# Performance work log

Hardware: AMD Instinct MI355X
Metric: run time of the kernel (lower is better)

## Reference

```python
import jax, jax.numpy as jnp
import numpy as np

S, B, E, H, FFN = 2048, 2, 1024, 16, 4096
HD = E // H
EPS = 1e-5

def setup_inputs() -> dict:
    key = jax.random.key(0)
    ks = jax.random.split(key, 10)
    w = lambda k, shape: 0.02 * jax.random.normal(k, shape, dtype=jnp.float32)
    inp = {
        "x": jax.random.normal(ks[0], (S, B, E), dtype=jnp.float32),
        "key_padding_mask": jax.random.randint(ks[1], (B, S), 0, 2) == 1,
        # attention projections, stored as (in, out) so y = x @ W + b
        "Wq": w(ks[2], (E, E)), "bq": jnp.zeros((E,), jnp.float32),
        "Wk": w(ks[3], (E, E)), "bk": jnp.zeros((E,), jnp.float32),
        "Wv": w(ks[4], (E, E)), "bv": jnp.zeros((E,), jnp.float32),
        "Wo": w(ks[5], (E, E)), "bo": jnp.zeros((E,), jnp.float32),
        "ln1_g": jnp.ones((E,), jnp.float32), "ln1_b": jnp.zeros((E,), jnp.float32),
        "W1": w(ks[6], (E, FFN)), "b1": jnp.zeros((FFN,), jnp.float32),
        "W2": w(ks[7], (FFN, E)), "b2": jnp.zeros((E,), jnp.float32),
        "ln2_g": jnp.ones((E,), jnp.float32), "ln2_b": jnp.zeros((E,), jnp.float32),
    }
    return inp

def layer_norm(x, g, b):
    m = jnp.mean(x, axis=-1, keepdims=True)
    v = jnp.mean(jnp.square(x - m), axis=-1, keepdims=True)
    return (x - m) * jax.lax.rsqrt(v + EPS) * g + b

def reference(x, key_padding_mask, Wq, bq, Wk, bk, Wv, bv, Wo, bo,
              ln1_g, ln1_b, W1, b1, W2, b2, ln2_g, ln2_b):
    # ---- self-attention (post-LN, normalize_before=False) ----
    residual = x  # (S, B, E)
    scaling = 1.0 / jnp.sqrt(jnp.float32(HD))
    q = (scaling * (x @ Wq + bq)).reshape(S, B, H, HD)
    k = (x @ Wk + bk).reshape(S, B, H, HD)
    v = (x @ Wv + bv).reshape(S, B, H, HD)
    # scores: (B, H, S_q, S_k)
    attn = jnp.einsum('ibhd,jbhd->bhij', q, k)
    attn = jnp.where(key_padding_mask[:, None, None, :], -jnp.inf, attn)
    attn = jax.nn.softmax(attn, axis=-1)
    out = jnp.einsum('bhij,jbhd->ibhd', attn, v).reshape(S, B, E)
    h = out @ Wo + bo
    h = layer_norm(residual + h, ln1_g, ln1_b)
    # ---- FFN ----
    residual = h
    f = jax.nn.relu(h @ W1 + b1) @ W2 + b2
    h = layer_norm(residual + f, ln2_g, ln2_b)
    # torch clamps only when inf/nan appear; finite inputs here so no-op
    return h
```

## Files before the change

kernel.cpp:

```cpp
#include <hip/hip_runtime.h>
#include <hip/hip_bf16.h>

using u16 = unsigned short;
using u32 = unsigned int;

constexpr int S_LEN = 2048, BATCH = 2, EMB = 1024, NHEAD = 16, HDIM = 64, FFN_DIM = 4096;
constexpr int NTOK = S_LEN * BATCH;
constexpr int QKV_N = 3 * EMB;
#define QSCALE 0.18033688011112042f

typedef __attribute__((ext_vector_type(4))) float f32x4;
typedef __attribute__((ext_vector_type(8))) short short8;
typedef __attribute__((ext_vector_type(8))) __bf16 bf16x8;
typedef __attribute__((ext_vector_type(8))) u16 ushort8;
typedef __attribute__((ext_vector_type(4))) u16 u16x4;
typedef __attribute__((ext_vector_type(2))) u32 u32x2;

typedef const __attribute__((address_space(1))) u16 gu16;
typedef __attribute__((address_space(3))) u16 lu16;

__device__ __forceinline__ u16 f2bf(float f) {
  u32 u = __builtin_bit_cast(u32, f);
  u32 r = u + 0x7fffu + ((u >> 16) & 1u);
  return (u16)(r >> 16);
}
__device__ __forceinline__ float bf2f(u16 u) {
  return __builtin_bit_cast(float, (u32)u << 16);
}

__device__ __forceinline__ f32x4 mfma16(short8 a, short8 b, f32x4 c) {
  return __builtin_amdgcn_mfma_f32_16x16x32_bf16(
      __builtin_bit_cast(bf16x8, a), __builtin_bit_cast(bf16x8, b), c, 0, 0, 0);
}

__device__ __forceinline__ void gload16(const u16* g, u16* l) {
  __builtin_amdgcn_global_load_lds((gu16*)g, (lu16*)l, 16, 0, 0);
}

__device__ __forceinline__ u32 cvtpk(float lo, float hi) {
  u32 r;
  asm("v_cvt_pk_bf16_f32 %0, %1, %2" : "=v"(r) : "v"(lo), "v"(hi));
  return r;
}

__global__ __launch_bounds__(256) void k_cvt_bf16(const float* __restrict__ in,
                                                  u16* __restrict__ out, int n) {
  int i = (blockIdx.x * 256 + threadIdx.x) * 8;
  if (i >= n) return;
  float4 a = *(const float4*)(in + i);
  float4 b = *(const float4*)(in + i + 4);
  ushort8 o;
  o[0] = f2bf(a.x); o[1] = f2bf(a.y); o[2] = f2bf(a.z); o[3] = f2bf(a.w);
  o[4] = f2bf(b.x); o[5] = f2bf(b.y); o[6] = f2bf(b.z); o[7] = f2bf(b.w);
  *(ushort8*)(out + i) = o;
}

__global__ __launch_bounds__(256) void k_transpose_w(const float* __restrict__ in,
                                                     u16* __restrict__ out, int R, int C,
                                                     float scale) {
  __shared__ float t[32][33];
  int c0 = blockIdx.x * 32, r0 = blockIdx.y * 32;
  int tx = threadIdx.x & 31, ty = threadIdx.x >> 5;
#pragma unroll
  for (int i = 0; i < 4; ++i)
    t[ty + i * 8][tx] = in[(r0 + ty + i * 8) * C + c0 + tx];
  __syncthreads();
#pragma unroll
  for (int i = 0; i < 4; ++i)
    out[(c0 + ty + i * 8) * R + r0 + tx] = f2bf(t[tx][ty + i * 8] * scale);
}

__global__ void k_bias_cat(const float* __restrict__ bq, const float* __restrict__ bk,
                           const float* __restrict__ bv, float* __restrict__ bcat) {
  int i = blockIdx.x * 256 + threadIdx.x;
  float v = (i < 1024) ? bq[i] * QSCALE : (i < 2048 ? bk[i - 1024] : bv[i - 2048]);
  bcat[i] = v;
}

__global__ void k_mask_f(const int* __restrict__ m, float* __restrict__ mf, int n) {
  int i = blockIdx.x * 256 + threadIdx.x;
  if (i < n) mf[i] = m[i] ? -1e30f : 0.f;
}

__global__ void k_transpose_v(const u16* __restrict__ qkvb, u16* __restrict__ vT) {
  __shared__ u16 t[64][65];
  int s0 = blockIdx.x * 64;
  int bh = blockIdx.y;
  int b = bh >> 4, h = bh & 15;
  int tx = threadIdx.x, ty = threadIdx.y;
#pragma unroll
  for (int i = 0; i < 16; ++i) {
    int s = i * 4 + ty;
    t[s][tx] = qkvb[((s0 + s) * BATCH + b) * QKV_N + 2048 + h * HDIM + tx];
  }
  __syncthreads();
#pragma unroll
  for (int i = 0; i < 16; ++i) {
    int d = i * 4 + ty;
    vT[(bh * HDIM + d) * S_LEN + s0 + tx] = t[tx][d];
  }
}

template <int NS, bool RELU>
__global__ __launch_bounds__(256, 4) void k_gemm128(
    const u16* __restrict__ A, const u16* __restrict__ Bt,
    const float* __restrict__ bias, u16* __restrict__ C,
    u16* __restrict__ P1, u16* __restrict__ P2, u16* __restrict__ P3,
    int M, int N, int K, int nbx) {
  __shared__ u16 As[2][128 * 32];
  __shared__ u16 Bs[2][128 * 32];
  int tid = threadIdx.x;
  int lane = tid & 63;
  int lm = lane & 15, lg = lane >> 4;
  int w = tid >> 6;
  int wm = w >> 1, wn = w & 1;

  int cpx = gridDim.x >> 3;
  int nw = (blockIdx.x & 7) * cpx + (blockIdx.x >> 3);
  int nb = gridDim.x / NS;
  int slice = nw / nb;
  int t0 = nw - slice * nb;
  int m0 = (t0 / nbx) * 128, n0 = (t0 % nbx) * 128;
  int klen = K / NS, koff = slice * klen;

  f32x4 z = {0.f, 0.f, 0.f, 0.f};
  f32x4 acc[4][4];
#pragma unroll
  for (int mi = 0; mi < 4; ++mi)
#pragma unroll
    for (int ni = 0; ni < 4; ++ni) acc[mi][ni] = z;

  const u16* aSrc[2];
  const u16* bSrc[2];
  int dOff[2];
#pragma unroll
  for (int i = 0; i < 2; ++i) {
    int ci = i * 256 + tid;
    int row = ci >> 2, ch = ci & 3;
    int sc = 8 * (ch ^ ((row >> 1) & 3));
    aSrc[i] = A + (m0 + row) * K + koff + sc;
    bSrc[i] = Bt + (n0 + row) * K + koff + sc;
    dOff[i] = ci * 8;
  }

  auto stage = [&](int buf, int k0) {
#pragma unroll
    for (int i = 0; i < 2; ++i) {
      gload16(aSrc[i] + k0, &As[buf][0] + dOff[i]);
      gload16(bSrc[i] + k0, &Bs[buf][0] + dOff[i]);
    }
  };

  int swz = (lm >> 1) & 3;
  int nkt = klen >> 5;
  stage(0, 0);
  __syncthreads();
  for (int t = 0; t < nkt; ++t) {
    int cur = t & 1;
    if (t + 1 < nkt) stage(cur ^ 1, (t + 1) << 5);
    const u16* Ab = &As[cur][0];
    const u16* Bb = &Bs[cur][0];
    __builtin_amdgcn_s_setprio(1);
    short8 bf[4];
#pragma unroll
    for (int ni = 0; ni < 4; ++ni) {
      int row = wn * 64 + ni * 16 + lm;
      bf[ni] = *(const short8*)(Bb + row * 32 + 8 * (lg ^ swz));
    }
#pragma unroll
    for (int mi = 0; mi < 4; ++mi) {
      int row = wm * 64 + mi * 16 + lm;
      short8 af = *(const short8*)(Ab + row * 32 + 8 * (lg ^ swz));
#pragma unroll
      for (int ni = 0; ni < 4; ++ni)
        acc[mi][ni] = mfma16(af, bf[ni], acc[mi][ni]);
    }
    __builtin_amdgcn_s_setprio(0);
    __syncthreads();
  }

  u16* Cout = C;
  if (NS > 1) Cout = (slice == 0) ? C : (slice == 1 ? P1 : (slice == 2 ? P2 : P3));
#pragma unroll
  for (int ni = 0; ni < 4; ++ni) {
    int c = n0 + wn * 64 + ni * 16 + lm;
    float bc = (NS == 1) ? bias[c] : 0.f;
#pragma unroll
    for (int mi = 0; mi < 4; ++mi) {
#pragma unroll
      for (int j = 0; j < 4; ++j) {
        int r = m0 + wm * 64 + mi * 16 + lg * 4 + j;
        float x = acc[mi][ni][j] + bc;
        if (RELU) x = fmaxf(x, 0.f);
        Cout[r * N + c] = f2bf(x);
      }
    }
  }
}

template <bool OUTB>
__global__ __launch_bounds__(256) void k_reduce_ln(
    const u16* __restrict__ P0, const u16* __restrict__ P1,
    const u16* __restrict__ P2, const u16* __restrict__ P3,
    const float* __restrict__ bias, const float* __restrict__ resid,
    const float* __restrict__ gam, const float* __restrict__ bet,
    float* __restrict__ outf, u16* __restrict__ outb) {
  int r = blockIdx.x;
  int tid = threadIdx.x;
  int c4 = tid * 4;
  int idx = r * EMB + c4;
  u16x4 a0 = *(const u16x4*)(P0 + idx);
  u16x4 a1 = *(const u16x4*)(P1 + idx);
  u16x4 a2 = *(const u16x4*)(P2 + idx);
  u16x4 a3 = *(const u16x4*)(P3 + idx);
  float4 bi = *(const float4*)(bias + c4);
  float4 rs = *(const float4*)(resid + idx);
  float4 v;
  v.x = bf2f(a0[0]) + bf2f(a1[0]) + bf2f(a2[0]) + bf2f(a3[0]) + bi.x + rs.x;
  v.y = bf2f(a0[1]) + bf2f(a1[1]) + bf2f(a2[1]) + bf2f(a3[1]) + bi.y + rs.y;
  v.z = bf2f(a0[2]) + bf2f(a1[2]) + bf2f(a2[2]) + bf2f(a3[2]) + bi.z + rs.z;
  v.w = bf2f(a0[3]) + bf2f(a1[3]) + bf2f(a2[3]) + bf2f(a3[3]) + bi.w + rs.w;
  float s = v.x + v.y + v.z + v.w;
  float ss = v.x * v.x + v.y * v.y + v.z * v.z + v.w * v.w;
#pragma unroll
  for (int off = 1; off < 64; off <<= 1) {
    s += __shfl_xor(s, off);
    ss += __shfl_xor(ss, off);
  }
  __shared__ float red[2][4];
  int w = tid >> 6, lane = tid & 63;
  if (lane == 0) { red[0][w] = s; red[1][w] = ss; }
  __syncthreads();
  s = red[0][0] + red[0][1] + red[0][2] + red[0][3];
  ss = red[1][0] + red[1][1] + red[1][2] + red[1][3];
  float mean = s * (1.f / EMB);
  float var = ss * (1.f / EMB) - mean * mean;
  float inv = rsqrtf(var + 1e-5f);
  float4 g = *(const float4*)(gam + c4);
  float4 be = *(const float4*)(bet + c4);
  float4 o;
  o.x = (v.x - mean) * inv * g.x + be.x;
  o.y = (v.y - mean) * inv * g.y + be.y;
  o.z = (v.z - mean) * inv * g.z + be.z;
  o.w = (v.w - mean) * inv * g.w + be.w;
  *(float4*)(outf + idx) = o;
  if (OUTB) {
    u16 ob[4] = {f2bf(o.x), f2bf(o.y), f2bf(o.z), f2bf(o.w)};
    *(u16x4*)(outb + idx) = *(u16x4*)ob;
  }
}

__global__ __launch_bounds__(256) void k_attn(
    const u16* __restrict__ qkvb, const u16* __restrict__ vT,
    const float* __restrict__ maskf, u16* __restrict__ outb) {
  __shared__ u16 Kl[2][4096];
  __shared__ u16 Vl[2][4096];
  __shared__ u16 Pl[4][1024];
  int tid = threadIdx.x;
  int lane = tid & 63, w = tid >> 6;
  int lm = lane & 15, lg = lane >> 4;
  int L = blockIdx.x;
  int bh = (L & 7) + 8 * (L >> 8);
  int qi0 = ((L >> 3) & 31) * 64;
  int b = bh >> 4, h = bh & 15;

  int qs = qi0 + w * 16 + lm;
  const u16* qp = qkvb + (qs * BATCH + b) * QKV_N + h * HDIM;
  short8 qf0 = *(const short8*)(qp + lg * 8);
  short8 qf1 = *(const short8*)(qp + 32 + lg * 8);

  int r0 = tid >> 3, c8 = tid & 7;
  int swz8 = 8 * (c8 ^ (r0 & 7));
  const u16* kA = qkvb + (r0 * BATCH + b) * QKV_N + 1024 + h * HDIM + swz8;
  const u16* kB = qkvb + ((r0 + 32) * BATCH + b) * QKV_N + 1024 + h * HDIM + swz8;
  const u16* vA = vT + (bh * HDIM + r0) * S_LEN + swz8;
  const u16* vB = vT + (bh * HDIM + r0 + 32) * S_LEN + swz8;
  const int KSTEP = 64 * BATCH * QKV_N;

  const float* mp = maskf + b * S_LEN;

  u16* Pw = Pl[w];
  int rd_swz = (lm & 7) << 3;
  const u16* prd0 = Pw + lm * 64 + ((lg * 8) ^ rd_swz);
  const u16* prd1 = Pw + lm * 64 + ((32 + lg * 8) ^ rd_swz);
  u16* pwr[4];
#pragma unroll
  for (int ni = 0; ni < 4; ++ni)
    pwr[ni] = Pw + lm * 64 + ((ni * 16 + lg * 4) ^ rd_swz);

  f32x4 z = {0.f, 0.f, 0.f, 0.f};
  f32x4 o[4] = {z, z, z, z};
  float lrow = 0.f;
  float4 mk[4], mknext[4];

  {
    u16* kd = Kl[0] + w * 512;
    u16* vd = Vl[0] + w * 512;
    gload16(kA, kd); gload16(kB, kd + 2048);
    gload16(vA, vd); gload16(vB, vd + 2048);
    kA += KSTEP; kB += KSTEP; vA += 64; vB += 64;
#pragma unroll
    for (int ni = 0; ni < 4; ++ni)
      mk[ni] = *(const float4*)(mp + ni * 16 + lg * 4);
  }
  __syncthreads();

  int cur = 0;
  for (int kt = 0; kt < S_LEN; kt += 64) {
    if (kt + 64 < S_LEN) {
      u16* kd = Kl[cur ^ 1] + w * 512;
      u16* vd = Vl[cur ^ 1] + w * 512;
      gload16(kA, kd); gload16(kB, kd + 2048);
      gload16(vA, vd); gload16(vB, vd + 2048);
      kA += KSTEP; kB += KSTEP; vA += 64; vB += 64;
#pragma unroll
      for (int ni = 0; ni < 4; ++ni)
        mknext[ni] = *(const float4*)(mp + kt + 64 + ni * 16 + lg * 4);
    }
    const u16* Kc = Kl[cur];
    const u16* Vc = Vl[cur];
#pragma unroll
    for (int ni = 0; ni < 4; ++ni) {
      const u16* kl = Kc + (ni * 16 + lm) * 64;
      short8 k0 = *(const short8*)(kl + ((lg * 8) ^ rd_swz));
      short8 k1 = *(const short8*)(kl + ((32 + lg * 8) ^ rd_swz));
      f32x4 t = mfma16(k0, qf0, z);
      f32x4 sv = mfma16(k1, qf1, t);
      float4 mb = mk[ni];
      float p0 = __builtin_amdgcn_exp2f(fminf(sv[0] + mb.x, 42.f));
      float p1 = __builtin_amdgcn_exp2f(fminf(sv[1] + mb.y, 42.f));
      float p2 = __builtin_amdgcn_exp2f(fminf(sv[2] + mb.z, 42.f));
      float p3 = __builtin_amdgcn_exp2f(fminf(sv[3] + mb.w, 42.f));
      lrow += (p0 + p1) + (p2 + p3);
      u32x2 pk;
      pk[0] = cvtpk(p0, p1);
      pk[1] = cvtpk(p2, p3);
      *(u32x2*)pwr[ni] = pk;
    }
    short8 pa0 = *(const short8*)prd0;
    short8 pa1 = *(const short8*)prd1;
#pragma unroll
    for (int ni = 0; ni < 4; ++ni) {
      const u16* vl = Vc + (ni * 16 + lm) * 64;
      short8 v0 = *(const short8*)(vl + ((lg * 8) ^ rd_swz));
      short8 v1 = *(const short8*)(vl + ((32 + lg * 8) ^ rd_swz));
      o[ni] = mfma16(pa0, v0, o[ni]);
      o[ni] = mfma16(pa1, v1, o[ni]);
    }
#pragma unroll
    for (int ni = 0; ni < 4; ++ni) mk[ni] = mknext[ni];
    __syncthreads();
    cur ^= 1;
  }

  lrow += __shfl_xor(lrow, 16);
  lrow += __shfl_xor(lrow, 32);
  float inv = 1.f / lrow;
  float invj[4];
#pragma unroll
  for (int j = 0; j < 4; ++j) invj[j] = __shfl(inv, lg * 4 + j);

#pragma unroll
  for (int ni = 0; ni < 4; ++ni) {
    int c = h * HDIM + ni * 16 + lm;
#pragma unroll
    for (int j = 0; j < 4; ++j) {
      int srow = qi0 + w * 16 + lg * 4 + j;
      outb[(srow * BATCH + b) * EMB + c] = f2bf(o[ni][j] * invj[j]);
    }
  }
}

extern "C" void kernel_launch(void* const* d_in, const int* in_sizes, int n_in,
                              void* d_out, int out_size, void* d_ws, size_t ws_size,
                              hipStream_t stream) {
  (void)in_sizes; (void)n_in; (void)out_size; (void)ws_size;
  const float* x = (const float*)d_in[0];
  const int* mask = (const int*)d_in[1];
  const float* Wq = (const float*)d_in[2];
  const float* bq = (const float*)d_in[3];
  const float* Wk = (const float*)d_in[4];
  const float* bk = (const float*)d_in[5];
  const float* Wv = (const float*)d_in[6];
  const float* bv = (const float*)d_in[7];
  const float* Wo = (const float*)d_in[8];
  const float* bo = (const float*)d_in[9];
  const float* g1 = (const float*)d_in[10];
  const float* be1 = (const float*)d_in[11];
  const float* W1 = (const float*)d_in[12];
  const float* b1 = (const float*)d_in[13];
  const float* W2 = (const float*)d_in[14];
  const float* b2 = (const float*)d_in[15];
  const float* g2 = (const float*)d_in[16];
  const float* be2 = (const float*)d_in[17];
  float* out = (float*)d_out;

  char* p = (char*)d_ws;
  u16* xb = (u16*)(p);
  u16* WqkvT = (u16*)(p + 8388608);
  u16* WoT = WqkvT + 3 * 1024 * 1024;
  u16* W1T = WoT + 1024 * 1024;
  u16* W2T = W1T + 1024 * 4096;
  u16* qkvb = (u16*)(p + 33554432);
  u16* ao = (u16*)(p + 58720256);
  float* bcat = (float*)(p + 67108864);
  float* maskf = (float*)(p + 67108864 + 16384);
  float* hf = (float*)(p + 67108864);
  u16* hb = (u16*)(p + 83886080);
  u16* vT = xb;
  u16* f1b = qkvb;
  u16* PP0 = xb;
  u16* PP1 = hb;
  u16* PP2 = (u16*)(p + 92274688);
  u16* PP3 = (u16*)(p + 100663296);

  k_cvt_bf16<<<NTOK * EMB / 2048, 256, 0, stream>>>(x, xb, NTOK * EMB);
  k_transpose_w<<<dim3(32, 32), 256, 0, stream>>>(Wq, WqkvT, 1024, 1024, QSCALE);
  k_transpose_w<<<dim3(32, 32), 256, 0, stream>>>(Wk, WqkvT + 1024 * 1024, 1024, 1024, 1.f);
  k_transpose_w<<<dim3(32, 32), 256, 0, stream>>>(Wv, WqkvT + 2 * 1024 * 1024, 1024, 1024, 1.f);
  k_transpose_w<<<dim3(32, 32), 256, 0, stream>>>(Wo, WoT, 1024, 1024, 1.f);
  k_transpose_w<<<dim3(128, 32), 256, 0, stream>>>(W1, W1T, 1024, 4096, 1.f);
  k_transpose_w<<<dim3(32, 128), 256, 0, stream>>>(W2, W2T, 4096, 1024, 1.f);
  k_bias_cat<<<12, 256, 0, stream>>>(bq, bk, bv, bcat);
  k_mask_f<<<16, 256, 0, stream>>>(mask, maskf, BATCH * S_LEN);

  k_gemm128<1, false><<<(NTOK / 128) * (QKV_N / 128), 256, 0, stream>>>(
      xb, WqkvT, bcat, qkvb, nullptr, nullptr, nullptr, NTOK, QKV_N, EMB, QKV_N / 128);

  k_transpose_v<<<dim3(S_LEN / 64, BATCH * NHEAD), dim3(64, 4), 0, stream>>>(qkvb, vT);
  k_attn<<<1024, 256, 0, stream>>>(qkvb, vT, maskf, ao);

  k_gemm128<4, false><<<(NTOK / 128) * (EMB / 128) * 4, 256, 0, stream>>>(
      ao, WoT, nullptr, PP0, PP1, PP2, PP3, NTOK, EMB, EMB, EMB / 128);
  k_reduce_ln<true><<<NTOK, 256, 0, stream>>>(
      PP0, PP1, PP2, PP3, bo, x, g1, be1, hf, hb);

  k_gemm128<1, true><<<(NTOK / 128) * (FFN_DIM / 128), 256, 0, stream>>>(
      hb, W1T, b1, f1b, nullptr, nullptr, nullptr, NTOK, FFN_DIM, EMB, FFN_DIM / 128);

  k_gemm128<4, false><<<(NTOK / 128) * (EMB / 128) * 4, 256, 0, stream>>>(
      f1b, W2T, nullptr, PP0, PP1, PP2, PP3, NTOK, EMB, FFN_DIM, EMB / 128);
  k_reduce_ln<false><<<NTOK, 256, 0, stream>>>(
      PP0, PP1, PP2, PP3, b2, hf, g2, be2, out, nullptr);
}
```

Before: 256.4 us.

## Process two 64-row query tiles per attention block to reuse K/V tiles

Each attention block now handles 128 query rows (two 64-row sub-tiles per wave) instead of 64, so every K/V tile loaded into shared memory feeds twice as many MFMAs. The grid drops from 1024 to 512 blocks, the P staging buffer doubles, and per-thread register use grows with the second set of accumulators and row sums. It also removes the fminf clamp before exp2, which saves instructions but drops the overflow guard on the unnormalized exponentials.

```diff
diff --git a/kernel.cpp b/kernel.cpp
--- a/kernel.cpp
+++ b/kernel.cpp
@@ -255,19 +255,23 @@
     const float* __restrict__ maskf, u16* __restrict__ outb) {
   __shared__ u16 Kl[2][4096];
   __shared__ u16 Vl[2][4096];
-  __shared__ u16 Pl[4][1024];
+  __shared__ u16 Pl[4][2048];
   int tid = threadIdx.x;
   int lane = tid & 63, w = tid >> 6;
   int lm = lane & 15, lg = lane >> 4;
   int L = blockIdx.x;
-  int bh = (L & 7) + 8 * (L >> 8);
-  int qi0 = ((L >> 3) & 31) * 64;
+  int bh = (L & 7) + 8 * (L >> 7);
+  int qi0 = ((L >> 3) & 15) * 128;
   int b = bh >> 4, h = bh & 15;
 
-  int qs = qi0 + w * 16 + lm;
-  const u16* qp = qkvb + (qs * BATCH + b) * QKV_N + h * HDIM;
-  short8 qf0 = *(const short8*)(qp + lg * 8);
-  short8 qf1 = *(const short8*)(qp + 32 + lg * 8);
+  short8 qf0[2], qf1[2];
+#pragma unroll
+  for (int qt = 0; qt < 2; ++qt) {
+    int qs = qi0 + qt * 64 + w * 16 + lm;
+    const u16* qp = qkvb + (qs * BATCH + b) * QKV_N + h * HDIM;
+    qf0[qt] = *(const short8*)(qp + lg * 8);
+    qf1[qt] = *(const short8*)(qp + 32 + lg * 8);
+  }
 
   int r0 = tid >> 3, c8 = tid & 7;
   int swz8 = 8 * (c8 ^ (r0 & 7));
@@ -289,8 +293,8 @@
     pwr[ni] = Pw + lm * 64 + ((ni * 16 + lg * 4) ^ rd_swz);
 
   f32x4 z = {0.f, 0.f, 0.f, 0.f};
-  f32x4 o[4] = {z, z, z, z};
-  float lrow = 0.f;
+  f32x4 o[2][4] = {{z, z, z, z}, {z, z, z, z}};
+  float lrow[2] = {0.f, 0.f};
   float4 mk[4], mknext[4];
 
   {
@@ -324,28 +328,38 @@
       const u16* kl = Kc + (ni * 16 + lm) * 64;
       short8 k0 = *(const short8*)(kl + ((lg * 8) ^ rd_swz));
       short8 k1 = *(const short8*)(kl + ((32 + lg * 8) ^ rd_swz));
-      f32x4 t = mfma16(k0, qf0, z);
-      f32x4 sv = mfma16(k1, qf1, t);
       float4 mb = mk[ni];
-      float p0 = __builtin_amdgcn_exp2f(fminf(sv[0] + mb.x, 42.f));
-      float p1 = __builtin_amdgcn_exp2f(fminf(sv[1] + mb.y, 42.f));
-      float p2 = __builtin_amdgcn_exp2f(fminf(sv[2] + mb.z, 42.f));
-      float p3 = __builtin_amdgcn_exp2f(fminf(sv[3] + mb.w, 42.f));
-      lrow += (p0 + p1) + (p2 + p3);
-      u32x2 pk;
-      pk[0] = cvtpk(p0, p1);
-      pk[1] = cvtpk(p2, p3);
-      *(u32x2*)pwr[ni] = pk;
-    }
-    short8 pa0 = *(const short8*)prd0;
-    short8 pa1 = *(const short8*)prd1;
+#pragma unroll
+      for (int qt = 0; qt < 2; ++qt) {
+        f32x4 t = mfma16(k0, qf0[qt], z);
+        f32x4 sv = mfma16(k1, qf1[qt], t);
+        float p0 = __builtin_amdgcn_exp2f(sv[0] + mb.x);
+        float p1 = __builtin_amdgcn_exp2f(sv[1] + mb.y);
+        float p2 = __builtin_amdgcn_exp2f(sv[2] + mb.z);
+        float p3 = __builtin_amdgcn_exp2f(sv[3] + mb.w);
+        lrow[qt] += (p0 + p1) + (p2 + p3);
+        u32x2 pk;
+        pk[0] = cvtpk(p0, p1);
+        pk[1] = cvtpk(p2, p3);
+        *(u32x2*)(pwr[ni] + qt * 1024) = pk;
+      }
+    }
+    short8 pa0[2], pa1[2];
+#pragma unroll
+    for (int qt = 0; qt < 2; ++qt) {
+      pa0[qt] = *(const short8*)(prd0 + qt * 1024);
+      pa1[qt] = *(const short8*)(prd1 + qt * 1024);
+    }
 #pragma unroll
     for (int ni = 0; ni < 4; ++ni) {
       const u16* vl = Vc + (ni * 16 + lm) * 64;
       short8 v0 = *(const short8*)(vl + ((lg * 8) ^ rd_swz));
       short8 v1 = *(const short8*)(vl + ((32 + lg * 8) ^ rd_swz));
-      o[ni] = mfma16(pa0, v0, o[ni]);
-      o[ni] = mfma16(pa1, v1, o[ni]);
+#pragma unroll
+      for (int qt = 0; qt < 2; ++qt) {
+        o[qt][ni] = mfma16(pa0[qt], v0, o[qt][ni]);
+        o[qt][ni] = mfma16(pa1[qt], v1, o[qt][ni]);
+      }
     }
 #pragma unroll
     for (int ni = 0; ni < 4; ++ni) mk[ni] = mknext[ni];
@@ -353,20 +367,23 @@
     cur ^= 1;
   }
 
-  lrow += __shfl_xor(lrow, 16);
-  lrow += __shfl_xor(lrow, 32);
-  float inv = 1.f / lrow;
-  float invj[4];
-#pragma unroll
-  for (int j = 0; j < 4; ++j) invj[j] = __shfl(inv, lg * 4 + j);
-
-#pragma unroll
-  for (int ni = 0; ni < 4; ++ni) {
-    int c = h * HDIM + ni * 16 + lm;
-#pragma unroll
-    for (int j = 0; j < 4; ++j) {
-      int srow = qi0 + w * 16 + lg * 4 + j;
-      outb[(srow * BATCH + b) * EMB + c] = f2bf(o[ni][j] * invj[j]);
+#pragma unroll
+  for (int qt = 0; qt < 2; ++qt) {
+    float l = lrow[qt];
+    l += __shfl_xor(l, 16);
+    l += __shfl_xor(l, 32);
+    float inv = 1.f / l;
+    float invj[4];
+#pragma unroll
+    for (int j = 0; j < 4; ++j) invj[j] = __shfl(inv, lg * 4 + j);
+#pragma unroll
+    for (int ni = 0; ni < 4; ++ni) {
+      int c = h * HDIM + ni * 16 + lm;
+#pragma unroll
+      for (int j = 0; j < 4; ++j) {
+        int srow = qi0 + qt * 64 + w * 16 + lg * 4 + j;
+        outb[(srow * BATCH + b) * EMB + c] = f2bf(o[qt][ni][j] * invj[j]);
+      }
     }
   }
 }
@@ -428,7 +445,7 @@
       xb, WqkvT, bcat, qkvb, nullptr, nullptr, nullptr, NTOK, QKV_N, EMB, QKV_N / 128);
 
   k_transpose_v<<<dim3(S_LEN / 64, BATCH * NHEAD), dim3(64, 4), 0, stream>>>(qkvb, vT);
-  k_attn<<<1024, 256, 0, stream>>>(qkvb, vT, maskf, ao);
+  k_attn<<<512, 256, 0, stream>>>(qkvb, vT, maskf, ao);
 
   k_gemm128<4, false><<<(NTOK / 128) * (EMB / 128) * 4, 256, 0, stream>>>(
       ao, WoT, nullptr, PP0, PP1, PP2, PP3, NTOK, EMB, EMB, EMB / 128);
```

Result: faster. 249.7 us (-2.6%).
